# Optimization experiments

Hardware: AMD Instinct MI355X
Metric: run time of the kernel (lower is better)

## Reference

```python
import jax, jax.numpy as jnp
import numpy as np

GRID = (8, 8, 8)    # grid_size
BLOCK = (4, 8, 8)   # block_size
EPS = 1e-5


def _block(x, ps):
    # x: (n,c,d,h,w) -> (n,c, gd*gh*gw, fd*fh*fw)
    n, c, d, h, w = x.shape
    gd, gh, gw = d // ps[0], h // ps[1], w // ps[2]
    x = x.reshape(n, c, gd, ps[0], gh, ps[1], gw, ps[2])
    x = x.transpose(0, 1, 2, 4, 6, 3, 5, 7)  # n,c,gd,gh,gw,fd,fh,fw
    return x.reshape(n, c, gd * gh * gw, ps[0] * ps[1] * ps[2])


def _unblock(x, gs, ps):
    # x: (n,c,G,P) -> (n,c, gd*fd, gh*fh, gw*fw)
    n, c, G, P = x.shape
    x = x.reshape(n, c, gs[0], gs[1], gs[2], ps[0], ps[1], ps[2])
    x = x.transpose(0, 1, 2, 5, 3, 6, 4, 7)
    return x.reshape(n, c, gs[0] * ps[0], gs[1] * ps[1], gs[2] * ps[2])


def setup_inputs() -> dict:
    key = jax.random.key(0)
    ks = jax.random.split(key, 9)
    c = 64
    G = GRID[0] * GRID[1] * GRID[2]    # 512
    P = BLOCK[0] * BLOCK[1] * BLOCK[2]  # 256
    x = jax.random.normal(ks[0], (4, c, 32, 64, 64), jnp.float32)
    def lin(k, fan_out, fan_in):
        s = 1.0 / np.sqrt(fan_in)
        kw, kb = jax.random.split(k)
        W = jax.random.uniform(kw, (fan_out, fan_in), jnp.float32, -s, s)
        b = jax.random.uniform(kb, (fan_out,), jnp.float32, -s, s)
        return W, b
    W1, b1 = lin(ks[1], 2 * c, c)
    W2, b2 = lin(ks[2], G, G)
    W3, b3 = lin(ks[3], P, P)
    W4, b4 = lin(ks[4], c, 2 * c)
    return {"x": x, "W1": W1, "b1": b1, "W2": W2, "b2": b2,
            "W3": W3, "b3": b3, "W4": W4, "b4": b4}


def reference(x, W1, b1, W2, b2, W3, b3, W4, b4):
    n, c, d, h, w = x.shape
    # LayerNorm over (c,d,h,w); affine params are freshly-initialized ones/zeros
    mu = x.mean(axis=(1, 2, 3, 4), keepdims=True)
    var = x.var(axis=(1, 2, 3, 4), keepdims=True)
    x = (x - mu) * jax.lax.rsqrt(var + EPS)
    # linear1 over channel dim (swapaxes+Linear+swapaxes == channel einsum)
    x = jnp.einsum('ncdhw,kc->nkdhw', x, W1) + b1[None, :, None, None, None]
    x = jax.nn.gelu(x, approximate=False)  # torch F.gelu default is exact erf
    u, v = jnp.split(x, 2, axis=1)
    # u: grid-mixing MLP over G = gd*gh*gw tokens
    gd, gh, gw = GRID
    pu = (d // gd, h // gh, w // gw)
    u = _block(u, pu)                                    # (n,c,G,Pu)
    u = jnp.einsum('ncgp,kg->nckp', u, W2) + b2[None, None, :, None]
    u = _unblock(u, GRID, pu)
    # v: block-mixing MLP over P = fd*fh*fw tokens
    fd, fh, fw = BLOCK
    gv = (d // fd, h // fh, w // fw)
    v = _block(v, BLOCK)                                 # (n,c,Gv,P)
    v = jnp.einsum('ncgp,kp->ncgk', v, W3) + b3
    v = _unblock(v, gv, BLOCK)
    x = jnp.concatenate([u, v], axis=1)                  # (n,2c,d,h,w)
    x = jnp.einsum('ncdhw,kc->nkdhw', x, W4) + b4[None, :, None, None, None]
    return x
```

## Files before the change

### kernel.cpp

```cpp
#include <hip/hip_runtime.h>
#include <hip/hip_bf16.h>
#include <math.h>


#define S_PER_N 131072
#define CNT_PER_N 8388608.0f

typedef __attribute__((ext_vector_type(8))) short bf16x8;
typedef __attribute__((ext_vector_type(4))) float f32x4;

__device__ __forceinline__ float b2f(unsigned short u) {
    return __uint_as_float(((unsigned int)u) << 16);
}
__device__ __forceinline__ unsigned short f2b(float f) {
    unsigned int i = __float_as_uint(f);
    unsigned int r = i + 0x7FFFu + ((i >> 16) & 1u);
    return (unsigned short)(r >> 16);
}
__device__ __forceinline__ float loadIn(const void* p, long i, bool f32) {
    return f32 ? ((const float*)p)[i] : b2f(((const unsigned short*)p)[i]);
}
__device__ __forceinline__ void storeOut(void* p, long i, float v, bool f32) {
    if (f32) ((float*)p)[i] = v;
    else ((unsigned short*)p)[i] = f2b(v);
}
__device__ __forceinline__ void gld16(const unsigned short* g, unsigned short* l) {
    __builtin_amdgcn_global_load_lds(
        (const __attribute__((address_space(1))) void*)g,
        (__attribute__((address_space(3))) void*)l,
        16, 0, 0);
}
__device__ __forceinline__ float fast_gelu(float x) {
    const float ax = fabsf(x);
    const float xs = x * 0.70710678118654752440f;
    const float axs = ax * 0.70710678118654752440f;
    const float t = __builtin_amdgcn_rcpf(1.0f + 0.3275911f * axs);
    float poly = 1.061405429f;
    poly = poly * t - 1.453152027f;
    poly = poly * t + 1.421413741f;
    poly = poly * t - 0.284496736f;
    poly = poly * t + 0.254829592f;
    const float e = __expf(-xs * xs);
    float erf_a = 1.0f - poly * t * e;
    erf_a = (x < 0.0f) ? -erf_a : erf_a;
    return 0.5f * x * (1.0f + erf_a);
}


__global__ void k_detect(const unsigned short* __restrict__ xw, float* __restrict__ flag) {
    __shared__ int sh[256];
    int tid = threadIdx.x;
    int sane = 0;
    for (int i = tid; i < 4096; i += 256) {
        int e = (xw[i] >> 7) & 0xFF;
        sane += (e >= 110 && e <= 130) ? 1 : 0;
    }
    sh[tid] = sane; __syncthreads();
    for (int off = 128; off; off >>= 1) {
        if (tid < off) sh[tid] += sh[tid + off];
        __syncthreads();
    }
    if (tid == 0) flag[0] = (sh[0] >= 3300) ? 0.0f : 1.0f;
}

__global__ __launch_bounds__(256) void k_lnstats(const void* __restrict__ xp,
                                                 const float* __restrict__ flag,
                                                 float* __restrict__ partials) {
    const bool f32 = flag[0] > 0.5f;
    const int bid = blockIdx.x;
    const long base = (long)bid * 65536;
    float s = 0.0f, sq = 0.0f;
    if (f32) {
        const float4* xv = (const float4*)((const float*)xp + base);
        for (int it = 0; it < 64; ++it) {
            float4 v = xv[it * 256 + threadIdx.x];
            s  += v.x + v.y + v.z + v.w;
            sq += v.x*v.x + v.y*v.y + v.z*v.z + v.w*v.w;
        }
    } else {
        const uint4* xv = (const uint4*)((const unsigned short*)xp + base);
        for (int it = 0; it < 32; ++it) {
            uint4 v = xv[it * 256 + threadIdx.x];
            unsigned int ws4[4] = {v.x, v.y, v.z, v.w};
            #pragma unroll
            for (int q = 0; q < 4; ++q) {
                float f0 = b2f((unsigned short)(ws4[q] & 0xFFFFu));
                float f1 = b2f((unsigned short)(ws4[q] >> 16));
                s += f0 + f1;
                sq += f0 * f0 + f1 * f1;
            }
        }
    }
    __shared__ float ls[256], lq[256];
    ls[threadIdx.x] = s; lq[threadIdx.x] = sq;
    __syncthreads();
    for (int off = 128; off > 0; off >>= 1) {
        if (threadIdx.x < off) {
            ls[threadIdx.x] += ls[threadIdx.x + off];
            lq[threadIdx.x] += lq[threadIdx.x + off];
        }
        __syncthreads();
    }
    if (threadIdx.x == 0) {
        partials[bid * 2 + 0] = ls[0];
        partials[bid * 2 + 1] = lq[0];
    }
}

__global__ void k_lnreduce(const float* __restrict__ partials, float* __restrict__ stats) {
    const int t = threadIdx.x;
    if (t < 4) {
        float s = 0.0f, sq = 0.0f;
        for (int i = 0; i < 128; ++i) {
            s  += partials[(t * 128 + i) * 2 + 0];
            sq += partials[(t * 128 + i) * 2 + 1];
        }
        stats[t * 2 + 0] = s;
        stats[t * 2 + 1] = sq;
    }
}

__global__ void k_prep(const void* __restrict__ W1, const void* __restrict__ b1,
                       const float* __restrict__ stats, const float* __restrict__ flag,
                       float* __restrict__ ck) {
    const bool f32 = flag[0] > 0.5f;
    const int k = threadIdx.x;
    float rs = 0.0f;
    for (int c = 0; c < 64; ++c) rs += loadIn(W1, (long)k * 64 + c, f32);
    const float bb = loadIn(b1, k, f32);
    for (int n = 0; n < 4; ++n) {
        const float mu   = stats[n * 2 + 0] * (1.0f / CNT_PER_N);
        const float m2   = stats[n * 2 + 1] * (1.0f / CNT_PER_N);
        const float rstd = rsqrtf(m2 - mu * mu + 1e-5f);
        ck[n * 128 + k] = bb - rstd * mu * rs;
    }
}

__global__ __launch_bounds__(256) void k_prepW(const void* __restrict__ W1,
                                               const void* __restrict__ W2,
                                               const void* __restrict__ W3,
                                               const void* __restrict__ W4,
                                               const float* __restrict__ flag,
                                               unsigned short* __restrict__ W1b,
                                               unsigned short* __restrict__ W2b,
                                               unsigned short* __restrict__ W3b,
                                               unsigned short* __restrict__ W4b) {
    const bool f32 = flag[0] > 0.5f;
    const int i = blockIdx.x * 256 + threadIdx.x;
    if (i < 512 * 512) W2b[i] = f32 ? f2b(((const float*)W2)[i]) : ((const unsigned short*)W2)[i];
    if (i < 256 * 256) W3b[i] = f32 ? f2b(((const float*)W3)[i]) : ((const unsigned short*)W3)[i];
    if (i < 128 * 64)  W1b[i] = f32 ? f2b(((const float*)W1)[i]) : ((const unsigned short*)W1)[i];
    if (i < 64 * 128)  W4b[i] = f32 ? f2b(((const float*)W4)[i]) : ((const unsigned short*)W4)[i];
}

__device__ __forceinline__ bf16x8 fragLd(const unsigned short* lds, int r, int c) {
    return *(const bf16x8*)&lds[r * 64 + ((c ^ (r & 7)) << 3)];
}

__global__ __launch_bounds__(256) void k_fc1_mfma(const void* __restrict__ xp,
                                                  const float* __restrict__ stats,
                                                  const float* __restrict__ ck,
                                                  const unsigned short* __restrict__ W1b,
                                                  const float* __restrict__ flag,
                                                  unsigned short* __restrict__ AuBase,
                                                  void* __restrict__ outBase, int nBase) {
    const bool f32 = flag[0] > 0.5f;
    __shared__ __align__(16) unsigned short Bs[256 * 64];
    const int nwg = gridDim.x;
    const int cpx = nwg >> 3;
    const int work = (blockIdx.x & 7) * cpx + (blockIdx.x >> 3);
    const int nl = work >> 9;
    const int n = nBase + nl;
    const int g = work & 511;
    const int d0 = (g >> 6) * 4, h0 = ((g >> 3) & 7) * 8, w0 = (g & 7) * 8;
    const int t = threadIdx.x;
    const int lane = t & 63, wid = t >> 6;
    const int waveP = wid * 64;
    const int lr = lane & 15, lk = lane >> 4;

    unsigned short* Au = AuBase + (size_t)nl * 8388608;
    unsigned short* Bv = (unsigned short*)((char*)outBase + (size_t)n * 8388608 * (f32 ? 4 : 2));

    {
        const int c0 = (t & 31) * 2;
        const int rdh = t >> 5;
        const long cbase = ((long)(n * 64 + c0)) << 17;
        const int ch = c0 >> 3, cof = c0 & 7;
        #pragma unroll
        for (int q = 0; q < 4; ++q) {
            const int dh = rdh * 4 + q;
            const int dp = dh >> 3, hp = dh & 7;
            const long sb = (long)(d0 + dp) * 4096 + (h0 + hp) * 64 + w0;
            unsigned short v0[8], v1[8];
            if (f32) {
                const float* r0 = (const float*)xp + cbase + sb;
                const float* r1 = r0 + S_PER_N;
                float4 a0 = *(const float4*)r0, a1 = *(const float4*)(r0 + 4);
                float4 b0 = *(const float4*)r1, b1v = *(const float4*)(r1 + 4);
                v0[0]=f2b(a0.x); v0[1]=f2b(a0.y); v0[2]=f2b(a0.z); v0[3]=f2b(a0.w);
                v0[4]=f2b(a1.x); v0[5]=f2b(a1.y); v0[6]=f2b(a1.z); v0[7]=f2b(a1.w);
                v1[0]=f2b(b0.x); v1[1]=f2b(b0.y); v1[2]=f2b(b0.z); v1[3]=f2b(b0.w);
                v1[4]=f2b(b1v.x); v1[5]=f2b(b1v.y); v1[6]=f2b(b1v.z); v1[7]=f2b(b1v.w);
            } else {
                const unsigned short* r0 = (const unsigned short*)xp + cbase + sb;
                uint4 a = *(const uint4*)r0;
                uint4 b = *(const uint4*)(r0 + S_PER_N);
                const unsigned short* pa = (const unsigned short*)&a;
                const unsigned short* pb = (const unsigned short*)&b;
                #pragma unroll
                for (int j = 0; j < 8; ++j) { v0[j] = pa[j]; v1[j] = pb[j]; }
            }
            const int pbase = dp * 64 + hp * 8;
            #pragma unroll
            for (int j = 0; j < 8; ++j) {
                const int pj = pbase + j;
                unsigned int val = (unsigned int)v0[j] | ((unsigned int)v1[j] << 16);
                *(unsigned int*)&Bs[pj * 64 + ((ch ^ (pj & 7)) << 3) + cof] = val;
            }
        }
    }
    __syncthreads();

    const float mu   = stats[n * 2 + 0] * (1.0f / CNT_PER_N);
    const float m2   = stats[n * 2 + 1] * (1.0f / CNT_PER_N);
    const float rstd = rsqrtf(m2 - mu * mu + 1e-5f);

    #pragma unroll
    for (int half = 0; half < 2; ++half) {
        f32x4 zero = {0.f, 0.f, 0.f, 0.f};
        f32x4 acc[4][4];
        #pragma unroll
        for (int i = 0; i < 4; ++i)
            #pragma unroll
            for (int j = 0; j < 4; ++j) acc[i][j] = zero;

        #pragma unroll
        for (int kk = 0; kk < 2; ++kk) {
            bf16x8 bp[4], aj[4];
            #pragma unroll
            for (int f = 0; f < 4; ++f) {
                bp[f] = fragLd(Bs, waveP + f * 16 + lr, kk * 4 + lk);
                aj[f] = *(const bf16x8*)(W1b + (long)(half * 64 + f * 16 + lr) * 64 + (kk * 4 + lk) * 8);
            }
            #pragma unroll
            for (int fp = 0; fp < 4; ++fp)
                #pragma unroll
                for (int fj = 0; fj < 4; ++fj)
                    acc[fp][fj] = __builtin_amdgcn_mfma_f32_16x16x32_bf16(bp[fp], aj[fj], acc[fp][fj], 0, 0, 0);
        }

        #pragma unroll
        for (int fj = 0; fj < 4; ++fj) {
            const int j = half * 64 + fj * 16 + lr;
            const float ckj = ck[n * 128 + j];
            #pragma unroll
            for (int fp = 0; fp < 4; ++fp) {
                const int pb = waveP + fp * 16 + lk * 4;
                unsigned short o[4];
                #pragma unroll
                for (int i = 0; i < 4; ++i) {
                    float v = acc[fp][fj][i] * rstd + ckj;
                    o[i] = f2b(fast_gelu(v));
                }
                uint2 pk;
                pk.x = (unsigned int)o[0] | ((unsigned int)o[1] << 16);
                pk.y = (unsigned int)o[2] | ((unsigned int)o[3] << 16);
                if (half == 0) {
                    *(uint2*)&Au[(long)j * S_PER_N + g * 256 + pb] = pk;
                } else {
                    *(uint2*)&Bv[((long)g * 64 + (j - 64)) * 256 + pb] = pk;
                }
            }
        }
    }
}

__global__ __launch_bounds__(256) void k_transA(const unsigned short* __restrict__ Abase,
                                                unsigned short* __restrict__ AtBase) {
    __shared__ unsigned short T[64 * 66];
    const int bid = blockIdx.x;
    const int nl = bid >> 11;
    const int inner = bid & 2047;
    const unsigned short* A = Abase + (size_t)nl * 8388608;
    unsigned short* At = AtBase + (size_t)nl * 8388608;
    const int c  = inner >> 5;
    const int gt = (inner >> 2) & 7, pt = inner & 3;
    const int g0 = gt * 64, p0 = pt * 64;
    const int t = threadIdx.x;

    const int gr = t >> 2, pc = (t & 3) * 16;
    const unsigned int* s32 = (const unsigned int*)(A + (long)c * S_PER_N + (long)(g0 + gr) * 256 + p0 + pc);
    unsigned int* d32 = (unsigned int*)&T[gr * 66 + pc];
    #pragma unroll
    for (int i = 0; i < 8; ++i) d32[i] = s32[i];
    __syncthreads();

    const int pr = t >> 2, gc0 = (t & 3) * 16;
    unsigned int ov[8];
    #pragma unroll
    for (int i = 0; i < 8; ++i) {
        unsigned int lo = T[(gc0 + 2 * i) * 66 + pr];
        unsigned int hi = T[(gc0 + 2 * i + 1) * 66 + pr];
        ov[i] = lo | (hi << 16);
    }
    unsigned int* dst = (unsigned int*)(At + ((long)(p0 + pr) * 64 + c) * 512 + g0 + gc0);
    #pragma unroll
    for (int i = 0; i < 8; ++i) dst[i] = ov[i];
}

__global__ __launch_bounds__(256) void k_umix_mfma(const unsigned short* __restrict__ BtBase,
                                                   const unsigned short* __restrict__ W2b,
                                                   const void* __restrict__ b2,
                                                   const float* __restrict__ flag,
                                                   unsigned short* __restrict__ TUBase) {
    const bool f32 = flag[0] > 0.5f;
    __shared__ __align__(16) unsigned short smem[17408];
    unsigned short* As = smem;
    unsigned short* Bs = smem + 8192;
    unsigned short* Ot = smem;
    const int bid = blockIdx.x;
    const int nl = bid >> 9;
    const int inner = bid & 511;
    const unsigned short* Bt = BtBase + (size_t)nl * 8388608;
    unsigned short* TU = TUBase + (size_t)nl * 8388608;
    const int mTile = inner >> 7;
    const int nTile = inner & 127;
    const int m0 = mTile * 128;
    const int t = threadIdx.x;
    const int lane = t & 63, wid = t >> 6;
    const int waveM = (wid >> 1) * 64, waveN = (wid & 1) * 64;
    const int lr = lane & 15, lk = lane >> 4;
    const int rIn8 = lane >> 3;
    const int swzOff = ((lane & 7) ^ rIn8) << 3;

    f32x4 zero = {0.f, 0.f, 0.f, 0.f};
    f32x4 acc[4][4];
    #pragma unroll
    for (int i = 0; i < 4; ++i)
        #pragma unroll
        for (int j = 0; j < 4; ++j) acc[i][j] = zero;

    for (int kb = 0; kb < 512; kb += 64) {
        #pragma unroll
        for (int call = 0; call < 4; ++call) {
            const int rowBase = call * 32 + wid * 8;
            gld16(W2b + (long)(m0 + rowBase + rIn8) * 512 + kb + swzOff, As + rowBase * 64);
            gld16(Bt + (long)(nTile * 128 + rowBase + rIn8) * 512 + kb + swzOff, Bs + rowBase * 64);
        }
        __syncthreads();
        #pragma unroll
        for (int kk = 0; kk < 2; ++kk) {
            bf16x8 tok[4], wf[4];
            #pragma unroll
            for (int f = 0; f < 4; ++f) {
                tok[f] = fragLd(Bs, waveN + f * 16 + lr, kk * 4 + lk);
                wf[f]  = fragLd(As, waveM + f * 16 + lr, kk * 4 + lk);
            }
            #pragma unroll
            for (int fm = 0; fm < 4; ++fm)
                #pragma unroll
                for (int fn = 0; fn < 4; ++fn)
                    acc[fm][fn] = __builtin_amdgcn_mfma_f32_16x16x32_bf16(tok[fm], wf[fn], acc[fm][fn], 0, 0, 0);
        }
        __syncthreads();
    }

    #pragma unroll
    for (int fn = 0; fn < 4; ++fn) {
        const int gp = waveM + fn * 16 + lr;
        const float bias = loadIn(b2, m0 + gp, f32);
        #pragma unroll
        for (int fm = 0; fm < 4; ++fm) {
            const int nb = waveN + fm * 16 + lk * 4;
            unsigned short o[4];
            #pragma unroll
            for (int i = 0; i < 4; ++i) o[i] = f2b(acc[fm][fn][i] + bias);
            uint2 pk;
            pk.x = (unsigned int)o[0] | ((unsigned int)o[1] << 16);
            pk.y = (unsigned int)o[2] | ((unsigned int)o[3] << 16);
            *(uint2*)&Ot[gp * 136 + nb] = pk;
        }
    }
    __syncthreads();
    {
        const int m = t >> 1, half = t & 1;
        const unsigned short* src = &Ot[m * 136 + half * 64];
        unsigned short* dst = TU + ((long)(m0 + m) * 256 + nTile * 2 + half) * 64;
        #pragma unroll
        for (int q = 0; q < 8; ++q)
            *(uint4*)(dst + q * 8) = *(const uint4*)(src + q * 8);
    }
}

__global__ __launch_bounds__(256) void k_vmix_mfma(void* __restrict__ outBase,
                                                   const unsigned short* __restrict__ W3b,
                                                   const void* __restrict__ b3,
                                                   const float* __restrict__ flag,
                                                   unsigned short* __restrict__ TVBase,
                                                   int nBase) {
    const bool f32 = flag[0] > 0.5f;
    __shared__ __align__(16) unsigned short smem[17408];
    unsigned short* As = smem;
    unsigned short* Bs = smem + 8192;
    unsigned short* Ot = smem;
    const int bid = blockIdx.x;
    const int nl = bid >> 9;
    const int n = nBase + nl;
    const int inner = bid & 511;
    const unsigned short* Bv = (const unsigned short*)((char*)outBase + (size_t)n * 8388608 * (f32 ? 4 : 2));
    unsigned short* TV = TVBase + (size_t)nl * 8388608;
    const int mTile = inner >> 8;
    const int nTile = inner & 255;
    const int m0 = mTile * 128;
    const int t = threadIdx.x;
    const int lane = t & 63, wid = t >> 6;
    const int waveM = (wid >> 1) * 64, waveN = (wid & 1) * 64;
    const int lr = lane & 15, lk = lane >> 4;
    const int rIn8 = lane >> 3;
    const int swzOff = ((lane & 7) ^ rIn8) << 3;

    f32x4 zero = {0.f, 0.f, 0.f, 0.f};
    f32x4 acc[4][4];
    #pragma unroll
    for (int i = 0; i < 4; ++i)
        #pragma unroll
        for (int j = 0; j < 4; ++j) acc[i][j] = zero;

    for (int kb = 0; kb < 256; kb += 64) {
        #pragma unroll
        for (int call = 0; call < 4; ++call) {
            const int rowBase = call * 32 + wid * 8;
            gld16(W3b + (long)(m0 + rowBase + rIn8) * 256 + kb + swzOff, As + rowBase * 64);
            gld16(Bv + (long)(nTile * 128 + rowBase + rIn8) * 256 + kb + swzOff, Bs + rowBase * 64);
        }
        __syncthreads();
        #pragma unroll
        for (int kk = 0; kk < 2; ++kk) {
            bf16x8 tok[4], wf[4];
            #pragma unroll
            for (int f = 0; f < 4; ++f) {
                tok[f] = fragLd(Bs, waveN + f * 16 + lr, kk * 4 + lk);
                wf[f]  = fragLd(As, waveM + f * 16 + lr, kk * 4 + lk);
            }
            #pragma unroll
            for (int fm = 0; fm < 4; ++fm)
                #pragma unroll
                for (int fn = 0; fn < 4; ++fn)
                    acc[fm][fn] = __builtin_amdgcn_mfma_f32_16x16x32_bf16(tok[fm], wf[fn], acc[fm][fn], 0, 0, 0);
        }
        __syncthreads();
    }

    #pragma unroll
    for (int fn = 0; fn < 4; ++fn) {
        const int kp = waveM + fn * 16 + lr;
        const float bias = loadIn(b3, m0 + kp, f32);
        #pragma unroll
        for (int fm = 0; fm < 4; ++fm) {
            const int nb = waveN + fm * 16 + lk * 4;
            unsigned short o[4];
            #pragma unroll
            for (int i = 0; i < 4; ++i) o[i] = f2b(acc[fm][fn][i] + bias);
            uint2 pk;
            pk.x = (unsigned int)o[0] | ((unsigned int)o[1] << 16);
            pk.y = (unsigned int)o[2] | ((unsigned int)o[3] << 16);
            *(uint2*)&Ot[kp * 136 + nb] = pk;
        }
    }
    __syncthreads();
    {
        const int m = t >> 1, half = t & 1;
        const unsigned short* src = &Ot[m * 136 + half * 64];
        unsigned short* dst = TV + ((long)(nTile * 2 + half) * 256 + m0 + m) * 64;
        #pragma unroll
        for (int q = 0; q < 8; ++q)
            *(uint4*)(dst + q * 8) = *(const uint4*)(src + q * 8);
    }
}

__global__ __launch_bounds__(256) void k_fc2_mfma(const unsigned short* __restrict__ TUBase,
                                                  const unsigned short* __restrict__ TVBase,
                                                  const unsigned short* __restrict__ W4b,
                                                  const void* __restrict__ b4,
                                                  const float* __restrict__ flag,
                                                  void* __restrict__ out, int nBase) {
    const bool f32 = flag[0] > 0.5f;
    const int bid = blockIdx.x;
    const int nl = bid >> 10;
    const int n = nBase + nl;
    const unsigned short* TU = TUBase + (size_t)nl * 8388608;
    const unsigned short* TV = TVBase + (size_t)nl * 8388608;
    const int s0 = (bid & 1023) * 128;
    const int t = threadIdx.x;
    const int lane = t & 63, wid = t >> 6;
    const int waveN = wid * 32;
    const int lr = lane & 15, lk = lane >> 4;

    long gpv[2];
    #pragma unroll
    for (int fn = 0; fn < 2; ++fn) {
        const int s = s0 + waveN + fn * 16 + lr;
        const int d = s >> 12, h = (s >> 6) & 63, w = s & 63;
        const int g = ((d >> 2) << 6) | ((h >> 3) << 3) | (w >> 3);
        const int p = ((d & 3) << 6) | ((h & 7) << 3) | (w & 7);
        gpv[fn] = (long)g * 256 + p;
    }

    f32x4 zero = {0.f, 0.f, 0.f, 0.f};
    f32x4 acc[4][2];
    #pragma unroll
    for (int i = 0; i < 4; ++i) { acc[i][0] = zero; acc[i][1] = zero; }

    #pragma unroll
    for (int kk = 0; kk < 4; ++kk) {
        const unsigned short* base = (kk < 2) ? TU : TV;
        const int choff = ((kk & 1) * 4 + lk) * 8;
        bf16x8 af[4], bfr[2];
        #pragma unroll
        for (int fm = 0; fm < 4; ++fm)
            af[fm] = *(const bf16x8*)(W4b + (long)(fm * 16 + lr) * 128 + (kk * 4 + lk) * 8);
        #pragma unroll
        for (int fn = 0; fn < 2; ++fn)
            bfr[fn] = *(const bf16x8*)(base + gpv[fn] * 64 + choff);
        #pragma unroll
        for (int fm = 0; fm < 4; ++fm)
            #pragma unroll
            for (int fn = 0; fn < 2; ++fn)
                acc[fm][fn] = __builtin_amdgcn_mfma_f32_16x16x32_bf16(af[fm], bfr[fn], acc[fm][fn], 0, 0, 0);
    }

    #pragma unroll
    for (int fm = 0; fm < 4; ++fm) {
        #pragma unroll
        for (int fn = 0; fn < 2; ++fn) {
            const int scol = s0 + waveN + fn * 16 + lr;
            #pragma unroll
            for (int i = 0; i < 4; ++i) {
                const int k = fm * 16 + lk * 4 + i;
                const float v = acc[fm][fn][i] + loadIn(b4, k, f32);
                storeOut(out, ((long)(n * 64 + k) << 17) + scol, v, f32);
            }
        }
    }
}

extern "C" void kernel_launch(void* const* d_in, const int* in_sizes, int n_in,
                              void* d_out, int out_size, void* d_ws, size_t ws_size,
                              hipStream_t stream) {
    const void* x  = d_in[0];
    const void* W1 = d_in[1];
    const void* b1 = d_in[2];
    const void* W2 = d_in[3];
    const void* b2 = d_in[4];
    const void* W3 = d_in[5];
    const void* b3 = d_in[6];
    const void* W4 = d_in[7];
    const void* b4 = d_in[8];

    float* wsf      = (float*)d_ws;
    float* stats    = wsf;
    float* flag     = wsf + 8;
    float* partials = wsf + 16;
    float* ck       = wsf + 1040;

    unsigned short* W2bf = (unsigned short*)((char*)d_ws + 8192);
    unsigned short* W3bf = W2bf + 512 * 512;
    unsigned short* W1bf = W3bf + 256 * 256;
    unsigned short* W4bf = W1bf + 128 * 64;

    const size_t perBuf = (size_t)8388608;
    const size_t need4  = (1u << 20) + 4ull * 2ull * perBuf * 2ull;
    const int cnt = (ws_size >= need4) ? 4 : 1;

    unsigned short* buf1 = (unsigned short*)((char*)d_ws + (1u << 20));
    unsigned short* buf2 = buf1 + (size_t)cnt * perBuf;

    hipLaunchKernelGGL(k_detect,   dim3(1),    dim3(256), 0, stream,
                       (const unsigned short*)x, flag);
    hipLaunchKernelGGL(k_lnstats,  dim3(512),  dim3(256), 0, stream, x, flag, partials);
    hipLaunchKernelGGL(k_lnreduce, dim3(1),    dim3(64),  0, stream, partials, stats);
    hipLaunchKernelGGL(k_prep,     dim3(1),    dim3(128), 0, stream, W1, b1, stats, flag, ck);
    hipLaunchKernelGGL(k_prepW,    dim3(1024), dim3(256), 0, stream,
                       W1, W2, W3, W4, flag, W1bf, W2bf, W3bf, W4bf);

    for (int nBase = 0; nBase < 4; nBase += cnt) {
        hipLaunchKernelGGL(k_fc1_mfma,  dim3(cnt * 512),  dim3(256), 0, stream,
                           x, stats, ck, W1bf, flag, buf2, d_out, nBase);
        hipLaunchKernelGGL(k_transA,    dim3(cnt * 2048), dim3(256), 0, stream, buf2, buf1);
        hipLaunchKernelGGL(k_umix_mfma, dim3(cnt * 512),  dim3(256), 0, stream,
                           buf1, W2bf, b2, flag, buf2);
        hipLaunchKernelGGL(k_vmix_mfma, dim3(cnt * 512),  dim3(256), 0, stream,
                           d_out, W3bf, b3, flag, buf1, nBase);
        hipLaunchKernelGGL(k_fc2_mfma,  dim3(cnt * 1024), dim3(256), 0, stream,
                           buf2, buf1, W4bf, b4, flag, d_out, nBase);
    }
}
```

Before: 336.6 us.

## Merge small prep kernels, co-schedule transpose with v-mix, use packed bf16 converts

Stats and weight-conversion kernels are folded into one launch, and the reduce and ck-prep kernels into another. The A-transpose and the v-branch block-mix GEMM now share one launch, split by block index, so independent work can overlap. A third workspace buffer holds the v-mix output. Manual bf16 rounding is replaced by the v_cvt_pk_bf16_f32 instruction, and the erf-polynomial GELU becomes a sigmoid/tanh-style approximation. Together these aim to cut launch overhead and ALU cost, in exchange for a larger workspace requirement (a smaller workspace falls back to per-batch loops) and a slightly different GELU approximation.

```diff
diff --git a/kernel.cpp b/kernel.cpp
--- a/kernel.cpp
+++ b/kernel.cpp
@@ -16,6 +16,11 @@
     unsigned int i = __float_as_uint(f);
     unsigned int r = i + 0x7FFFu + ((i >> 16) & 1u);
     return (unsigned short)(r >> 16);
+}
+__device__ __forceinline__ unsigned int pk2(float lo, float hi) {
+    unsigned int r;
+    asm("v_cvt_pk_bf16_f32 %0, %1, %2" : "=v"(r) : "v"(lo), "v"(hi));
+    return r;
 }
 __device__ __forceinline__ float loadIn(const void* p, long i, bool f32) {
     return f32 ? ((const float*)p)[i] : b2f(((const unsigned short*)p)[i]);
@@ -31,21 +36,12 @@
         16, 0, 0);
 }
 __device__ __forceinline__ float fast_gelu(float x) {
-    const float ax = fabsf(x);
-    const float xs = x * 0.70710678118654752440f;
-    const float axs = ax * 0.70710678118654752440f;
-    const float t = __builtin_amdgcn_rcpf(1.0f + 0.3275911f * axs);
-    float poly = 1.061405429f;
-    poly = poly * t - 1.453152027f;
-    poly = poly * t + 1.421413741f;
-    poly = poly * t - 0.284496736f;
-    poly = poly * t + 0.254829592f;
-    const float e = __expf(-xs * xs);
-    float erf_a = 1.0f - poly * t * e;
-    erf_a = (x < 0.0f) ? -erf_a : erf_a;
-    return 0.5f * x * (1.0f + erf_a);
-}
-
+    const float x2 = x * x;
+    const float c = -0.102944f * x2 - 2.3022081f;
+    const float q = x * c;
+    const float t = __builtin_amdgcn_rcpf(1.0f + __builtin_amdgcn_exp2f(q));
+    return x * t;
+}
 
 __global__ void k_detect(const unsigned short* __restrict__ xw, float* __restrict__ flag) {
     __shared__ int sh[256];
@@ -63,10 +59,26 @@
     if (tid == 0) flag[0] = (sh[0] >= 3300) ? 0.0f : 1.0f;
 }
 
-__global__ __launch_bounds__(256) void k_lnstats(const void* __restrict__ xp,
-                                                 const float* __restrict__ flag,
-                                                 float* __restrict__ partials) {
+__global__ __launch_bounds__(256) void k_stats_prepW(const void* __restrict__ xp,
+                                                     const float* __restrict__ flag,
+                                                     float* __restrict__ partials,
+                                                     const void* __restrict__ W1,
+                                                     const void* __restrict__ W2,
+                                                     const void* __restrict__ W3,
+                                                     const void* __restrict__ W4,
+                                                     unsigned short* __restrict__ W1b,
+                                                     unsigned short* __restrict__ W2b,
+                                                     unsigned short* __restrict__ W3b,
+                                                     unsigned short* __restrict__ W4b) {
     const bool f32 = flag[0] > 0.5f;
+    if (blockIdx.x >= 512) {
+        const int i = (blockIdx.x - 512) * 256 + threadIdx.x;
+        if (i < 512 * 512) W2b[i] = f32 ? f2b(((const float*)W2)[i]) : ((const unsigned short*)W2)[i];
+        if (i < 256 * 256) W3b[i] = f32 ? f2b(((const float*)W3)[i]) : ((const unsigned short*)W3)[i];
+        if (i < 128 * 64)  W1b[i] = f32 ? f2b(((const float*)W1)[i]) : ((const unsigned short*)W1)[i];
+        if (i < 64 * 128)  W4b[i] = f32 ? f2b(((const float*)W4)[i]) : ((const unsigned short*)W4)[i];
+        return;
+    }
     const int bid = blockIdx.x;
     const long base = (long)bid * 65536;
     float s = 0.0f, sq = 0.0f;
@@ -107,7 +119,9 @@
     }
 }
 
-__global__ void k_lnreduce(const float* __restrict__ partials, float* __restrict__ stats) {
+__global__ void k_red_prep(const float* __restrict__ partials, float* __restrict__ stats,
+                           const void* __restrict__ W1, const void* __restrict__ b1,
+                           const float* __restrict__ flag, float* __restrict__ ck) {
     const int t = threadIdx.x;
     if (t < 4) {
         float s = 0.0f, sq = 0.0f;
@@ -118,39 +132,17 @@
         stats[t * 2 + 0] = s;
         stats[t * 2 + 1] = sq;
     }
-}
-
-__global__ void k_prep(const void* __restrict__ W1, const void* __restrict__ b1,
-                       const float* __restrict__ stats, const float* __restrict__ flag,
-                       float* __restrict__ ck) {
+    __syncthreads();
     const bool f32 = flag[0] > 0.5f;
-    const int k = threadIdx.x;
     float rs = 0.0f;
-    for (int c = 0; c < 64; ++c) rs += loadIn(W1, (long)k * 64 + c, f32);
-    const float bb = loadIn(b1, k, f32);
+    for (int c = 0; c < 64; ++c) rs += loadIn(W1, (long)t * 64 + c, f32);
+    const float bb = loadIn(b1, t, f32);
     for (int n = 0; n < 4; ++n) {
         const float mu   = stats[n * 2 + 0] * (1.0f / CNT_PER_N);
         const float m2   = stats[n * 2 + 1] * (1.0f / CNT_PER_N);
         const float rstd = rsqrtf(m2 - mu * mu + 1e-5f);
-        ck[n * 128 + k] = bb - rstd * mu * rs;
-    }
-}
-
-__global__ __launch_bounds__(256) void k_prepW(const void* __restrict__ W1,
-                                               const void* __restrict__ W2,
-                                               const void* __restrict__ W3,
-                                               const void* __restrict__ W4,
-                                               const float* __restrict__ flag,
-                                               unsigned short* __restrict__ W1b,
-                                               unsigned short* __restrict__ W2b,
-                                               unsigned short* __restrict__ W3b,
-                                               unsigned short* __restrict__ W4b) {
-    const bool f32 = flag[0] > 0.5f;
-    const int i = blockIdx.x * 256 + threadIdx.x;
-    if (i < 512 * 512) W2b[i] = f32 ? f2b(((const float*)W2)[i]) : ((const unsigned short*)W2)[i];
-    if (i < 256 * 256) W3b[i] = f32 ? f2b(((const float*)W3)[i]) : ((const unsigned short*)W3)[i];
-    if (i < 128 * 64)  W1b[i] = f32 ? f2b(((const float*)W1)[i]) : ((const unsigned short*)W1)[i];
-    if (i < 64 * 128)  W4b[i] = f32 ? f2b(((const float*)W4)[i]) : ((const unsigned short*)W4)[i];
+        ck[n * 128 + t] = bb - rstd * mu * rs;
+    }
 }
 
 __device__ __forceinline__ bf16x8 fragLd(const unsigned short* lds, int r, int c) {
@@ -191,16 +183,19 @@
             const int dh = rdh * 4 + q;
             const int dp = dh >> 3, hp = dh & 7;
             const long sb = (long)(d0 + dp) * 4096 + (h0 + hp) * 64 + w0;
-            unsigned short v0[8], v1[8];
+            const int pbase = dp * 64 + hp * 8;
             if (f32) {
                 const float* r0 = (const float*)xp + cbase + sb;
                 const float* r1 = r0 + S_PER_N;
                 float4 a0 = *(const float4*)r0, a1 = *(const float4*)(r0 + 4);
                 float4 b0 = *(const float4*)r1, b1v = *(const float4*)(r1 + 4);
-                v0[0]=f2b(a0.x); v0[1]=f2b(a0.y); v0[2]=f2b(a0.z); v0[3]=f2b(a0.w);
-                v0[4]=f2b(a1.x); v0[5]=f2b(a1.y); v0[6]=f2b(a1.z); v0[7]=f2b(a1.w);
-                v1[0]=f2b(b0.x); v1[1]=f2b(b0.y); v1[2]=f2b(b0.z); v1[3]=f2b(b0.w);
-                v1[4]=f2b(b1v.x); v1[5]=f2b(b1v.y); v1[6]=f2b(b1v.z); v1[7]=f2b(b1v.w);
+                float ff0[8] = {a0.x, a0.y, a0.z, a0.w, a1.x, a1.y, a1.z, a1.w};
+                float ff1[8] = {b0.x, b0.y, b0.z, b0.w, b1v.x, b1v.y, b1v.z, b1v.w};
+                #pragma unroll
+                for (int j = 0; j < 8; ++j) {
+                    const int pj = pbase + j;
+                    *(unsigned int*)&Bs[pj * 64 + ((ch ^ (pj & 7)) << 3) + cof] = pk2(ff0[j], ff1[j]);
+                }
             } else {
                 const unsigned short* r0 = (const unsigned short*)xp + cbase + sb;
                 uint4 a = *(const uint4*)r0;
@@ -208,14 +203,11 @@
                 const unsigned short* pa = (const unsigned short*)&a;
                 const unsigned short* pb = (const unsigned short*)&b;
                 #pragma unroll
-                for (int j = 0; j < 8; ++j) { v0[j] = pa[j]; v1[j] = pb[j]; }
-            }
-            const int pbase = dp * 64 + hp * 8;
-            #pragma unroll
-            for (int j = 0; j < 8; ++j) {
-                const int pj = pbase + j;
-                unsigned int val = (unsigned int)v0[j] | ((unsigned int)v1[j] << 16);
-                *(unsigned int*)&Bs[pj * 64 + ((ch ^ (pj & 7)) << 3) + cof] = val;
+                for (int j = 0; j < 8; ++j) {
+                    const int pj = pbase + j;
+                    unsigned int val = (unsigned int)pa[j] | ((unsigned int)pb[j] << 16);
+                    *(unsigned int*)&Bs[pj * 64 + ((ch ^ (pj & 7)) << 3) + cof] = val;
+                }
             }
         }
     }
@@ -256,15 +248,13 @@
             #pragma unroll
             for (int fp = 0; fp < 4; ++fp) {
                 const int pb = waveP + fp * 16 + lk * 4;
-                unsigned short o[4];
-                #pragma unroll
-                for (int i = 0; i < 4; ++i) {
-                    float v = acc[fp][fj][i] * rstd + ckj;
-                    o[i] = f2b(fast_gelu(v));
-                }
+                float gg[4];
+                #pragma unroll
+                for (int i = 0; i < 4; ++i)
+                    gg[i] = fast_gelu(acc[fp][fj][i] * rstd + ckj);
                 uint2 pk;
-                pk.x = (unsigned int)o[0] | ((unsigned int)o[1] << 16);
-                pk.y = (unsigned int)o[2] | ((unsigned int)o[3] << 16);
+                pk.x = pk2(gg[0], gg[1]);
+                pk.y = pk2(gg[2], gg[3]);
                 if (half == 0) {
                     *(uint2*)&Au[(long)j * S_PER_N + g * 256 + pb] = pk;
                 } else {
@@ -275,37 +265,121 @@
     }
 }
 
-__global__ __launch_bounds__(256) void k_transA(const unsigned short* __restrict__ Abase,
-                                                unsigned short* __restrict__ AtBase) {
-    __shared__ unsigned short T[64 * 66];
-    const int bid = blockIdx.x;
-    const int nl = bid >> 11;
-    const int inner = bid & 2047;
-    const unsigned short* A = Abase + (size_t)nl * 8388608;
-    unsigned short* At = AtBase + (size_t)nl * 8388608;
-    const int c  = inner >> 5;
-    const int gt = (inner >> 2) & 7, pt = inner & 3;
-    const int g0 = gt * 64, p0 = pt * 64;
+__global__ __launch_bounds__(256) void k_tv(const unsigned short* __restrict__ AuBase,
+                                            void* __restrict__ outBase,
+                                            const unsigned short* __restrict__ W3b,
+                                            const void* __restrict__ b3,
+                                            const float* __restrict__ flag,
+                                            unsigned short* __restrict__ AtBase,
+                                            unsigned short* __restrict__ TVBase,
+                                            int nBase, int nV) {
+    __shared__ __align__(16) unsigned short smem[17408];
     const int t = threadIdx.x;
 
-    const int gr = t >> 2, pc = (t & 3) * 16;
-    const unsigned int* s32 = (const unsigned int*)(A + (long)c * S_PER_N + (long)(g0 + gr) * 256 + p0 + pc);
-    unsigned int* d32 = (unsigned int*)&T[gr * 66 + pc];
-    #pragma unroll
-    for (int i = 0; i < 8; ++i) d32[i] = s32[i];
-    __syncthreads();
-
-    const int pr = t >> 2, gc0 = (t & 3) * 16;
-    unsigned int ov[8];
-    #pragma unroll
-    for (int i = 0; i < 8; ++i) {
-        unsigned int lo = T[(gc0 + 2 * i) * 66 + pr];
-        unsigned int hi = T[(gc0 + 2 * i + 1) * 66 + pr];
-        ov[i] = lo | (hi << 16);
-    }
-    unsigned int* dst = (unsigned int*)(At + ((long)(p0 + pr) * 64 + c) * 512 + g0 + gc0);
-    #pragma unroll
-    for (int i = 0; i < 8; ++i) dst[i] = ov[i];
+    if ((int)blockIdx.x < nV) {
+        const bool f32 = flag[0] > 0.5f;
+        unsigned short* As = smem;
+        unsigned short* Bs = smem + 8192;
+        unsigned short* Ot = smem;
+        const int bid = blockIdx.x;
+        const int nl = bid >> 9;
+        const int n = nBase + nl;
+        const int inner = bid & 511;
+        const unsigned short* Bv = (const unsigned short*)((char*)outBase + (size_t)n * 8388608 * (f32 ? 4 : 2));
+        unsigned short* TV = TVBase + (size_t)nl * 8388608;
+        const int mTile = inner >> 8;
+        const int nTile = inner & 255;
+        const int m0 = mTile * 128;
+        const int lane = t & 63, wid = t >> 6;
+        const int waveM = (wid >> 1) * 64, waveN = (wid & 1) * 64;
+        const int lr = lane & 15, lk = lane >> 4;
+        const int rIn8 = lane >> 3;
+        const int swzOff = ((lane & 7) ^ rIn8) << 3;
+
+        f32x4 zero = {0.f, 0.f, 0.f, 0.f};
+        f32x4 acc[4][4];
+        #pragma unroll
+        for (int i = 0; i < 4; ++i)
+            #pragma unroll
+            for (int j = 0; j < 4; ++j) acc[i][j] = zero;
+
+        for (int kb = 0; kb < 256; kb += 64) {
+            #pragma unroll
+            for (int call = 0; call < 4; ++call) {
+                const int rowBase = call * 32 + wid * 8;
+                gld16(W3b + (long)(m0 + rowBase + rIn8) * 256 + kb + swzOff, As + rowBase * 64);
+                gld16(Bv + (long)(nTile * 128 + rowBase + rIn8) * 256 + kb + swzOff, Bs + rowBase * 64);
+            }
+            __syncthreads();
+            #pragma unroll
+            for (int kk = 0; kk < 2; ++kk) {
+                bf16x8 tok[4], wf[4];
+                #pragma unroll
+                for (int f = 0; f < 4; ++f) {
+                    tok[f] = fragLd(Bs, waveN + f * 16 + lr, kk * 4 + lk);
+                    wf[f]  = fragLd(As, waveM + f * 16 + lr, kk * 4 + lk);
+                }
+                #pragma unroll
+                for (int fm = 0; fm < 4; ++fm)
+                    #pragma unroll
+                    for (int fn = 0; fn < 4; ++fn)
+                        acc[fm][fn] = __builtin_amdgcn_mfma_f32_16x16x32_bf16(tok[fm], wf[fn], acc[fm][fn], 0, 0, 0);
+            }
+            __syncthreads();
+        }
+
+        #pragma unroll
+        for (int fn = 0; fn < 4; ++fn) {
+            const int kp = waveM + fn * 16 + lr;
+            const float bias = loadIn(b3, m0 + kp, f32);
+            #pragma unroll
+            for (int fm = 0; fm < 4; ++fm) {
+                const int nb = waveN + fm * 16 + lk * 4;
+                uint2 pk;
+                pk.x = pk2(acc[fm][fn][0] + bias, acc[fm][fn][1] + bias);
+                pk.y = pk2(acc[fm][fn][2] + bias, acc[fm][fn][3] + bias);
+                *(uint2*)&Ot[kp * 136 + nb] = pk;
+            }
+        }
+        __syncthreads();
+        {
+            const int m = t >> 1, half = t & 1;
+            const unsigned short* src = &Ot[m * 136 + half * 64];
+            unsigned short* dst = TV + ((long)(nTile * 2 + half) * 256 + m0 + m) * 64;
+            #pragma unroll
+            for (int q = 0; q < 8; ++q)
+                *(uint4*)(dst + q * 8) = *(const uint4*)(src + q * 8);
+        }
+    } else {
+        unsigned short* T = smem;
+        const int bid = blockIdx.x - nV;
+        const int nl = bid >> 11;
+        const int inner = bid & 2047;
+        const unsigned short* A = AuBase + (size_t)nl * 8388608;
+        unsigned short* At = AtBase + (size_t)nl * 8388608;
+        const int c  = inner >> 5;
+        const int gt = (inner >> 2) & 7, pt = inner & 3;
+        const int g0 = gt * 64, p0 = pt * 64;
+
+        const int gr = t >> 2, pc = (t & 3) * 16;
+        const unsigned int* s32 = (const unsigned int*)(A + (long)c * S_PER_N + (long)(g0 + gr) * 256 + p0 + pc);
+        unsigned int* d32 = (unsigned int*)&T[gr * 66 + pc];
+        #pragma unroll
+        for (int i = 0; i < 8; ++i) d32[i] = s32[i];
+        __syncthreads();
+
+        const int pr = t >> 2, gc0 = (t & 3) * 16;
+        unsigned int ov[8];
+        #pragma unroll
+        for (int i = 0; i < 8; ++i) {
+            unsigned int lo = T[(gc0 + 2 * i) * 66 + pr];
+            unsigned int hi = T[(gc0 + 2 * i + 1) * 66 + pr];
+            ov[i] = lo | (hi << 16);
+        }
+        unsigned int* dst = (unsigned int*)(At + ((long)(p0 + pr) * 64 + c) * 512 + g0 + gc0);
+        #pragma unroll
+        for (int i = 0; i < 8; ++i) dst[i] = ov[i];
+    }
 }
 
 __global__ __launch_bounds__(256) void k_umix_mfma(const unsigned short* __restrict__ BtBase,
@@ -372,12 +446,9 @@
         #pragma unroll
         for (int fm = 0; fm < 4; ++fm) {
             const int nb = waveN + fm * 16 + lk * 4;
-            unsigned short o[4];
-            #pragma unroll
-            for (int i = 0; i < 4; ++i) o[i] = f2b(acc[fm][fn][i] + bias);
             uint2 pk;
-            pk.x = (unsigned int)o[0] | ((unsigned int)o[1] << 16);
-            pk.y = (unsigned int)o[2] | ((unsigned int)o[3] << 16);
+            pk.x = pk2(acc[fm][fn][0] + bias, acc[fm][fn][1] + bias);
+            pk.y = pk2(acc[fm][fn][2] + bias, acc[fm][fn][3] + bias);
             *(uint2*)&Ot[gp * 136 + nb] = pk;
         }
     }
@@ -386,92 +457,6 @@
         const int m = t >> 1, half = t & 1;
         const unsigned short* src = &Ot[m * 136 + half * 64];
         unsigned short* dst = TU + ((long)(m0 + m) * 256 + nTile * 2 + half) * 64;
-        #pragma unroll
-        for (int q = 0; q < 8; ++q)
-            *(uint4*)(dst + q * 8) = *(const uint4*)(src + q * 8);
-    }
-}
-
-__global__ __launch_bounds__(256) void k_vmix_mfma(void* __restrict__ outBase,
-                                                   const unsigned short* __restrict__ W3b,
-                                                   const void* __restrict__ b3,
-                                                   const float* __restrict__ flag,
-                                                   unsigned short* __restrict__ TVBase,
-                                                   int nBase) {
-    const bool f32 = flag[0] > 0.5f;
-    __shared__ __align__(16) unsigned short smem[17408];
-    unsigned short* As = smem;
-    unsigned short* Bs = smem + 8192;
-    unsigned short* Ot = smem;
-    const int bid = blockIdx.x;
-    const int nl = bid >> 9;
-    const int n = nBase + nl;
-    const int inner = bid & 511;
-    const unsigned short* Bv = (const unsigned short*)((char*)outBase + (size_t)n * 8388608 * (f32 ? 4 : 2));
-    unsigned short* TV = TVBase + (size_t)nl * 8388608;
-    const int mTile = inner >> 8;
-    const int nTile = inner & 255;
-    const int m0 = mTile * 128;
-    const int t = threadIdx.x;
-    const int lane = t & 63, wid = t >> 6;
-    const int waveM = (wid >> 1) * 64, waveN = (wid & 1) * 64;
-    const int lr = lane & 15, lk = lane >> 4;
-    const int rIn8 = lane >> 3;
-    const int swzOff = ((lane & 7) ^ rIn8) << 3;
-
-    f32x4 zero = {0.f, 0.f, 0.f, 0.f};
-    f32x4 acc[4][4];
-    #pragma unroll
-    for (int i = 0; i < 4; ++i)
-        #pragma unroll
-        for (int j = 0; j < 4; ++j) acc[i][j] = zero;
-
-    for (int kb = 0; kb < 256; kb += 64) {
-        #pragma unroll
-        for (int call = 0; call < 4; ++call) {
-            const int rowBase = call * 32 + wid * 8;
-            gld16(W3b + (long)(m0 + rowBase + rIn8) * 256 + kb + swzOff, As + rowBase * 64);
-            gld16(Bv + (long)(nTile * 128 + rowBase + rIn8) * 256 + kb + swzOff, Bs + rowBase * 64);
-        }
-        __syncthreads();
-        #pragma unroll
-        for (int kk = 0; kk < 2; ++kk) {
-            bf16x8 tok[4], wf[4];
-            #pragma unroll
-            for (int f = 0; f < 4; ++f) {
-                tok[f] = fragLd(Bs, waveN + f * 16 + lr, kk * 4 + lk);
-                wf[f]  = fragLd(As, waveM + f * 16 + lr, kk * 4 + lk);
-            }
-            #pragma unroll
-            for (int fm = 0; fm < 4; ++fm)
-                #pragma unroll
-                for (int fn = 0; fn < 4; ++fn)
-                    acc[fm][fn] = __builtin_amdgcn_mfma_f32_16x16x32_bf16(tok[fm], wf[fn], acc[fm][fn], 0, 0, 0);
-        }
-        __syncthreads();
-    }
-
-    #pragma unroll
-    for (int fn = 0; fn < 4; ++fn) {
-        const int kp = waveM + fn * 16 + lr;
-        const float bias = loadIn(b3, m0 + kp, f32);
-        #pragma unroll
-        for (int fm = 0; fm < 4; ++fm) {
-            const int nb = waveN + fm * 16 + lk * 4;
-            unsigned short o[4];
-            #pragma unroll
-            for (int i = 0; i < 4; ++i) o[i] = f2b(acc[fm][fn][i] + bias);
-            uint2 pk;
-            pk.x = (unsigned int)o[0] | ((unsigned int)o[1] << 16);
-            pk.y = (unsigned int)o[2] | ((unsigned int)o[3] << 16);
-            *(uint2*)&Ot[kp * 136 + nb] = pk;
-        }
-    }
-    __syncthreads();
-    {
-        const int m = t >> 1, half = t & 1;
-        const unsigned short* src = &Ot[m * 136 + half * 64];
-        unsigned short* dst = TV + ((long)(nTile * 2 + half) * 256 + m0 + m) * 64;
         #pragma unroll
         for (int q = 0; q < 8; ++q)
             *(uint4*)(dst + q * 8) = *(const uint4*)(src + q * 8);
@@ -569,29 +554,28 @@
     unsigned short* W4bf = W1bf + 128 * 64;
 
     const size_t perBuf = (size_t)8388608;
-    const size_t need4  = (1u << 20) + 4ull * 2ull * perBuf * 2ull;
+    const size_t need4  = (1u << 20) + 3ull * 4ull * perBuf * 2ull;
     const int cnt = (ws_size >= need4) ? 4 : 1;
 
     unsigned short* buf1 = (unsigned short*)((char*)d_ws + (1u << 20));
     unsigned short* buf2 = buf1 + (size_t)cnt * perBuf;
-
-    hipLaunchKernelGGL(k_detect,   dim3(1),    dim3(256), 0, stream,
+    unsigned short* buf3 = buf2 + (size_t)cnt * perBuf;
+
+    hipLaunchKernelGGL(k_detect,      dim3(1),    dim3(256), 0, stream,
                        (const unsigned short*)x, flag);
-    hipLaunchKernelGGL(k_lnstats,  dim3(512),  dim3(256), 0, stream, x, flag, partials);
-    hipLaunchKernelGGL(k_lnreduce, dim3(1),    dim3(64),  0, stream, partials, stats);
-    hipLaunchKernelGGL(k_prep,     dim3(1),    dim3(128), 0, stream, W1, b1, stats, flag, ck);
-    hipLaunchKernelGGL(k_prepW,    dim3(1024), dim3(256), 0, stream,
-                       W1, W2, W3, W4, flag, W1bf, W2bf, W3bf, W4bf);
+    hipLaunchKernelGGL(k_stats_prepW, dim3(1536), dim3(256), 0, stream,
+                       x, flag, partials, W1, W2, W3, W4, W1bf, W2bf, W3bf, W4bf);
+    hipLaunchKernelGGL(k_red_prep,    dim3(1),    dim3(128), 0, stream,
+                       partials, stats, W1, b1, flag, ck);
 
     for (int nBase = 0; nBase < 4; nBase += cnt) {
         hipLaunchKernelGGL(k_fc1_mfma,  dim3(cnt * 512),  dim3(256), 0, stream,
                            x, stats, ck, W1bf, flag, buf2, d_out, nBase);
-        hipLaunchKernelGGL(k_transA,    dim3(cnt * 2048), dim3(256), 0, stream, buf2, buf1);
+        hipLaunchKernelGGL(k_tv,        dim3(cnt * 2560), dim3(256), 0, stream,
+                           buf2, d_out, W3bf, b3, flag, buf1, buf3, nBase, cnt * 512);
         hipLaunchKernelGGL(k_umix_mfma, dim3(cnt * 512),  dim3(256), 0, stream,
                            buf1, W2bf, b2, flag, buf2);
-        hipLaunchKernelGGL(k_vmix_mfma, dim3(cnt * 512),  dim3(256), 0, stream,
-                           d_out, W3bf, b3, flag, buf1, nBase);
         hipLaunchKernelGGL(k_fc2_mfma,  dim3(cnt * 1024), dim3(256), 0, stream,
-                           buf2, buf1, W4bf, b4, flag, d_out, nBase);
-    }
-}
+                           buf2, buf3, W4bf, b4, flag, d_out, nBase);
+    }
+}
```

Measured after the change: 337.5 us. About the same (+0.3%).
